# Performance work log

Measured on AMD Instinct MI355X. Metric: run time of the kernel, lower is better.

The kernel has to match this reference:

```python
import jax, jax.numpy as jnp
import numpy as np

B, N, D = 2, 256, 256  # module only type-checks when n_tokens == dim
EPS = 1e-5


def _ln(x, gamma, beta):
    m = jnp.mean(x, axis=-1, keepdims=True)
    v = jnp.var(x, axis=-1, keepdims=True)
    return (x - m) * jax.lax.rsqrt(v + EPS) * gamma + beta


def setup_inputs() -> dict:
    key = jax.random.key(0)
    k0, k1, k2, k3 = jax.random.split(key, 4)
    s = 1.0 / np.sqrt(D).astype(np.float32)
    return {
        "pair_repr": jax.random.normal(k0, (B, N, N, D), jnp.float32),
        "w_in": jax.random.normal(k1, (2 * D, D), jnp.float32) * s,
        "w_gate": jax.random.normal(k2, (D, D), jnp.float32) * s,
        "w_out": jax.random.normal(k3, (D, D), jnp.float32) * s,
        "ln_gamma": jnp.ones((D,), jnp.float32),
        "ln_beta": jnp.zeros((D,), jnp.float32),
    }


def reference(pair_repr, w_in, w_gate, w_out, ln_gamma, ln_beta):
    # shared LayerNorm applied to input
    x = _ln(pair_repr, ln_gamma, ln_beta)                      # [B,N,N,D]
    ab = jnp.einsum('bnid,ed->bnie', x, w_in)                  # [B,N,N,2D]
    a, b = jnp.split(ab, 2, axis=-1)
    a = jax.nn.sigmoid(a) * a                                  # SiLU
    b = jax.nn.sigmoid(b) * b
    g = jax.nn.sigmoid(jnp.einsum('bnid,ed->bnie', x, w_gate))  # [B,N,N,D]
    # 'incoming' pattern: torch.einsum('...ki,...kj->...ij') with ellipsis = (B, N);
    # contracts over the second token axis k, i/j index the channel axis (needs N == D).
    tri = jnp.einsum('bnki,bnkj->bnij', a, b)                  # [B,N,D,D]
    out = jnp.einsum('bnij,ej->bnie', _ln(tri, ln_gamma, ln_beta), w_out)
    return out * g
```

## Files before the change

kernel.cpp:

```cpp
#include <hip/hip_runtime.h>
#include <hip/hip_bf16.h>

typedef __attribute__((ext_vector_type(4))) float  f32x4;
typedef __attribute__((ext_vector_type(8))) short  s16x8;
typedef __attribute__((ext_vector_type(4))) short  s16x4;

union BH4 { s16x4 v; __hip_bfloat16 h[4]; };
union BH8 { s16x8 v; __hip_bfloat16 h[8]; };

#define MFMA16(A,B,C) __builtin_amdgcn_mfma_f32_16x16x32_bf16((A),(B),(C),0,0,0)

__device__ __forceinline__ float sigm(float x) { return 1.0f / (1.0f + __expf(-x)); }

__device__ __forceinline__ int xad(int r, int byteInRow) {
  return ((r << 9) + byteInRow) ^ ((r & 7) << 4);
}
__device__ __forceinline__ int cad64(int i, int k) {
  return (i << 7) + ((((k >> 3) ^ (i & 7)) << 4) | ((k & 7) << 1));
}

__global__ void wfrag_kernel(const float* __restrict__ w_in,
                             const float* __restrict__ w_gate,
                             const float* __restrict__ w_out,
                             __hip_bfloat16* __restrict__ dst) {
  const int lane = threadIdx.x;
  const int fid  = blockIdx.x;
  const int m    = blockIdx.y;
  const float* src = (m == 0) ? w_in : (m == 1) ? (w_in + 65536)
                    : (m == 2) ? w_gate : w_out;
  const int e  = (fid >> 3) * 16 + (lane & 15);
  const int d0 = (fid & 7) * 32 + (lane >> 4) * 8;
  BH8 u;
  #pragma unroll
  for (int j = 0; j < 8; ++j) u.h[j] = __float2bfloat16(src[e * 256 + d0 + j]);
  *reinterpret_cast<s16x8*>(dst + (size_t)m * 65536 + ((size_t)fid * 64 + lane) * 8) = u.v;
}

__global__ __launch_bounds__(512, 4) void k2_lnabg(
    const float* __restrict__ pair,
    const __hip_bfloat16* __restrict__ wfrag,
    const float* __restrict__ gamma, const float* __restrict__ beta,
    __hip_bfloat16* __restrict__ aT, __hip_bfloat16* __restrict__ bT,
    __hip_bfloat16* __restrict__ gws)
{
  __shared__ __align__(16) char lds[65536];
  const int raw = blockIdx.x;
  const int s   = (raw & 7) * 64 + (raw >> 3);
  const int tid = threadIdx.x, lane = tid & 63, w = tid >> 6;
  const int l15 = lane & 15, lh = lane >> 4;
  char* const XW = lds + w * 8192;

  const float4 gm = *reinterpret_cast<const float4*>(gamma + lane * 4);
  const float4 bt = *reinterpret_cast<const float4*>(beta  + lane * 4);

  s16x8 xr[2][8];
  #pragma unroll
  for (int rt = 0; rt < 2; ++rt) {
    #pragma unroll 1
    for (int rr = 0; rr < 16; ++rr) {
      const int r = w * 32 + rt * 16 + rr;
      const float4 v = *reinterpret_cast<const float4*>(
          pair + ((size_t)s * 256 + r) * 256 + lane * 4);
      float sm = v.x + v.y + v.z + v.w;
      float ss = v.x*v.x + v.y*v.y + v.z*v.z + v.w*v.w;
      #pragma unroll
      for (int m = 1; m < 64; m <<= 1) { sm += __shfl_xor(sm, m); ss += __shfl_xor(ss, m); }
      const float mean = sm * (1.f/256.f);
      const float rstd = rsqrtf(ss * (1.f/256.f) - mean*mean + 1e-5f);
      BH4 o;
      o.h[0] = __float2bfloat16((v.x - mean) * rstd * gm.x + bt.x);
      o.h[1] = __float2bfloat16((v.y - mean) * rstd * gm.y + bt.y);
      o.h[2] = __float2bfloat16((v.z - mean) * rstd * gm.z + bt.z);
      o.h[3] = __float2bfloat16((v.w - mean) * rstd * gm.w + bt.w);
      *reinterpret_cast<s16x4*>(XW + xad(rr, lane * 8)) = o.v;
    }
    #pragma unroll
    for (int ks = 0; ks < 8; ++ks)
      xr[rt][ks] = *reinterpret_cast<const s16x8*>(XW + xad(l15, ks*64 + lh*16));
  }

  #pragma unroll 1
  for (int cg = 0; cg < 48; ++cg) {
    const int m  = cg >> 4;
    const int ct = cg & 15;
    f32x4 acc0 = (f32x4){0.f,0.f,0.f,0.f};
    f32x4 acc1 = (f32x4){0.f,0.f,0.f,0.f};
    #pragma unroll
    for (int ks = 0; ks < 8; ++ks) {
      const s16x8 Bf = *reinterpret_cast<const s16x8*>(
          wfrag + ((size_t)cg * 8 + ks) * 512 + lane * 8);
      acc0 = MFMA16(xr[0][ks], Bf, acc0);
      acc1 = MFMA16(xr[1][ks], Bf, acc1);
    }
    if (m < 2) {
      __hip_bfloat16* const dst = (m == 0) ? aT : bT;
      #pragma unroll
      for (int rt = 0; rt < 2; ++rt) {
        const f32x4 a = rt ? acc1 : acc0;
        BH4 o;
        #pragma unroll
        for (int q = 0; q < 4; ++q) o.h[q] = __float2bfloat16(a[q] * sigm(a[q]));
        const int lane2 = l15 + 16 * ((rt*2 + (lh >> 1)) & 3);
        *reinterpret_cast<s16x4*>(
            dst + (((size_t)s*16 + ct)*8 + w)*512 + lane2*8 + (lh & 1)*4) = o.v;
      }
    } else {
      #pragma unroll
      for (int rt = 0; rt < 2; ++rt) {
        const f32x4 a = rt ? acc1 : acc0;
        BH4 o;
        #pragma unroll
        for (int q = 0; q < 4; ++q) o.h[q] = __float2bfloat16(sigm(a[q]));
        const int rtg = w * 2 + rt;
        *reinterpret_cast<s16x4*>(
            gws + (((size_t)s*16 + rtg)*16 + ct)*256 + lane*4) = o.v;
      }
    }
  }
}

__global__ __launch_bounds__(512, 4) void k3_tri(
    const __hip_bfloat16* __restrict__ aT, const __hip_bfloat16* __restrict__ bT,
    const __hip_bfloat16* __restrict__ gws, const __hip_bfloat16* __restrict__ wfrag,
    const float* __restrict__ gamma, const float* __restrict__ beta,
    float* __restrict__ out)
{
  extern __shared__ __align__(16) char lds[];
  char*  const STG = lds;
  char*  const SW  = lds;
  float* const ST  = (float*)(lds + 65536);

  const int raw = blockIdx.x;
  const int s   = (raw & 7) * 64 + ((raw >> 3) >> 1);
  const int h   = (raw >> 3) & 1;
  const int tid = threadIdx.x, lane = tid & 63, w = tid >> 6;
  const int l15 = lane & 15, lh = lane >> 4;
  const int r2 = w >> 1, ch = w & 1;

  f32x4 tri[2][8];
  #pragma unroll
  for (int rt = 0; rt < 2; ++rt)
    #pragma unroll
    for (int t = 0; t < 8; ++t) tri[rt][t] = (f32x4){0.f,0.f,0.f,0.f};

  const int f0 = w * 3;
  s16x8 stg[3];
  #pragma unroll
  for (int p = 0; p < 3; ++p) {
    const int f = f0 + p;
    const __hip_bfloat16* src = (f < 8)
        ? aT + (((size_t)s*16 + h*8 + f)*8 + 0)*512
        : bT + (((size_t)s*16 + (f-8))*8 + 0)*512;
    stg[p] = *reinterpret_cast<const s16x8*>(src + lane*8);
  }

  for (int c = 0; c < 8; ++c) {
    #pragma unroll
    for (int p = 0; p < 3; ++p)
      *reinterpret_cast<s16x8*>(STG + (f0 + p)*1024 + lane*16) = stg[p];
    __syncthreads();
    if (c < 7) {
      #pragma unroll
      for (int p = 0; p < 3; ++p) {
        const int f = f0 + p;
        const __hip_bfloat16* src = (f < 8)
            ? aT + (((size_t)s*16 + h*8 + f)*8 + (c+1))*512
            : bT + (((size_t)s*16 + (f-8))*8 + (c+1))*512;
        stg[p] = *reinterpret_cast<const s16x8*>(src + lane*8);
      }
    }
    const s16x8 ta0 = *reinterpret_cast<const s16x8*>(STG + (r2*2+0)*1024 + lane*16);
    const s16x8 ta1 = *reinterpret_cast<const s16x8*>(STG + (r2*2+1)*1024 + lane*16);
    #pragma unroll
    for (int t = 0; t < 8; ++t) {
      const s16x8 tb = *reinterpret_cast<const s16x8*>(
          STG + (8 + ch*8 + t)*1024 + lane*16);
      tri[0][t] = MFMA16(ta0, tb, tri[0][t]);
      tri[1][t] = MFMA16(ta1, tb, tri[1][t]);
    }
    __syncthreads();
  }

  float psm[2][4], pss[2][4];
  #pragma unroll
  for (int rt = 0; rt < 2; ++rt)
    #pragma unroll
    for (int q = 0; q < 4; ++q) {
      float sm = 0.f, ss = 0.f;
      #pragma unroll
      for (int t = 0; t < 8; ++t) { const float v = tri[rt][t][q]; sm += v; ss += v*v; }
      #pragma unroll
      for (int m = 1; m < 16; m <<= 1) { sm += __shfl_xor(sm, m); ss += __shfl_xor(ss, m); }
      psm[rt][q] = sm; pss[rt][q] = ss;
    }
  if (l15 == 0) {
    #pragma unroll
    for (int rt = 0; rt < 2; ++rt)
      #pragma unroll
      for (int q = 0; q < 4; ++q) {
        const int idx = ((w*2 + rt)*4 + lh)*4 + q;
        ST[idx*2 + 0] = psm[rt][q];
        ST[idx*2 + 1] = pss[rt][q];
      }
  }
  __syncthreads();
  float mean[2][4], rstd[2][4];
  #pragma unroll
  for (int rt = 0; rt < 2; ++rt)
    #pragma unroll
    for (int q = 0; q < 4; ++q) {
      const int idx = (((w ^ 1)*2 + rt)*4 + lh)*4 + q;
      const float sm = psm[rt][q] + ST[idx*2 + 0];
      const float ss = pss[rt][q] + ST[idx*2 + 1];
      mean[rt][q] = sm * (1.f/256.f);
      rstd[rt][q] = rsqrtf(ss * (1.f/256.f) - mean[rt][q]*mean[rt][q] + 1e-5f);
    }
  __syncthreads();
  #pragma unroll
  for (int t = 0; t < 8; ++t) {
    const int j = (ch*8 + t)*16 + l15;
    const float gmv = gamma[j], btv = beta[j];
    #pragma unroll
    for (int rt = 0; rt < 2; ++rt)
      #pragma unroll
      for (int q = 0; q < 4; ++q) {
        const int iloc = r2*32 + rt*16 + lh*4 + q;
        const float v = (tri[rt][t][q] - mean[rt][q]) * rstd[rt][q] * gmv + btv;
        *reinterpret_cast<__hip_bfloat16*>(SW + xad(iloc, j*2)) = __float2bfloat16(v);
      }
  }
  __syncthreads();

  const __hip_bfloat16* const wo = wfrag + 196608;
  f32x4 oo[2][8];
  #pragma unroll
  for (int rt = 0; rt < 2; ++rt)
    #pragma unroll
    for (int t = 0; t < 8; ++t) oo[rt][t] = (f32x4){0.f,0.f,0.f,0.f};
  #pragma unroll
  for (int ks = 0; ks < 8; ++ks) {
    const s16x8 A0 = *reinterpret_cast<const s16x8*>(
        SW + xad(r2*32 +  0 + l15, ks*64 + lh*16));
    const s16x8 A1 = *reinterpret_cast<const s16x8*>(
        SW + xad(r2*32 + 16 + l15, ks*64 + lh*16));
    #pragma unroll
    for (int t = 0; t < 8; ++t) {
      const int cte = ch*8 + t;
      const s16x8 Bo = *reinterpret_cast<const s16x8*>(
          wo + ((size_t)(cte*8 + ks))*512 + lane*8);
      oo[0][t] = MFMA16(A0, Bo, oo[0][t]);
      oo[1][t] = MFMA16(A1, Bo, oo[1][t]);
    }
  }
  #pragma unroll
  for (int rt = 0; rt < 2; ++rt) {
    const int rtg = h*8 + r2*2 + rt;
    #pragma unroll
    for (int t = 0; t < 8; ++t) {
      BH4 gv;
      gv.v = *reinterpret_cast<const s16x4*>(
          gws + (((size_t)s*16 + rtg)*16 + (ch*8 + t))*256 + lane*4);
      #pragma unroll
      for (int q = 0; q < 4; ++q) {
        const int row = h*128 + r2*32 + rt*16 + lh*4 + q;
        out[((size_t)s*256 + row)*256 + (ch*8 + t)*16 + l15] =
            oo[rt][t][q] * __bfloat162float(gv.h[q]);
      }
    }
  }
}

__global__ __launch_bounds__(256) void ln_kernel(
    const float* __restrict__ pair, const float* __restrict__ gamma,
    const float* __restrict__ beta, __hip_bfloat16* __restrict__ xws)
{
  __shared__ char Xl[8192];
  const int t  = threadIdx.x;
  const int s  = blockIdx.x >> 4;
  const int rt = blockIdx.x & 15;
  const int r  = t >> 4;
  const int c0 = (t & 15) * 16;
  const float* src = pair + (((size_t)s * 256 + rt * 16 + r) * 256 + c0);
  float v[16];
  #pragma unroll
  for (int i = 0; i < 4; ++i) {
    const float4 f = *reinterpret_cast<const float4*>(src + i * 4);
    v[i*4+0]=f.x; v[i*4+1]=f.y; v[i*4+2]=f.z; v[i*4+3]=f.w;
  }
  float sm = 0.f, ss = 0.f;
  #pragma unroll
  for (int i = 0; i < 16; ++i) { sm += v[i]; ss += v[i]*v[i]; }
  #pragma unroll
  for (int m = 1; m < 16; m <<= 1) { sm += __shfl_xor(sm, m); ss += __shfl_xor(ss, m); }
  const float mean = sm * (1.f/256.f);
  const float rstd = rsqrtf(ss * (1.f/256.f) - mean*mean + 1e-5f);
  #pragma unroll
  for (int i = 0; i < 4; ++i) {
    const float4 gm = *reinterpret_cast<const float4*>(gamma + c0 + i*4);
    const float4 bt = *reinterpret_cast<const float4*>(beta  + c0 + i*4);
    BH4 o;
    o.h[0] = __float2bfloat16((v[i*4+0]-mean)*rstd*gm.x + bt.x);
    o.h[1] = __float2bfloat16((v[i*4+1]-mean)*rstd*gm.y + bt.y);
    o.h[2] = __float2bfloat16((v[i*4+2]-mean)*rstd*gm.z + bt.z);
    o.h[3] = __float2bfloat16((v[i*4+3]-mean)*rstd*gm.w + bt.w);
    *reinterpret_cast<s16x4*>(Xl + xad(r, (c0 + i*4)*2)) = o.v;
  }
  __syncthreads();
  #pragma unroll
  for (int p = 0; p < 2; ++p) {
    const int u  = t + p * 256;
    const int ks = u >> 6;
    const int lp = u & 63;
    const s16x8 f = *reinterpret_cast<const s16x8*>(
        Xl + xad(lp & 15, ks*64 + ((lp>>4)&3)*16));
    *reinterpret_cast<s16x8*>(xws + ((((size_t)s*16 + rt)*8 + ks)*64 + lp)*8) = f;
  }
}

__global__ __launch_bounds__(512, 2) void tri_fused_fb(
    const __hip_bfloat16* __restrict__ xws,
    const __hip_bfloat16* __restrict__ wfrag,
    const float* __restrict__ gamma, const float* __restrict__ beta,
    float* __restrict__ out)
{
  extern __shared__ __align__(16) char lds[];
  char* const XS = lds;
  char* const AC = lds + 32768;
  char* const BC = lds + 49152;
  char* const SW = lds;

  const int raw = blockIdx.x;
  const int xcd = raw & 7, o = raw >> 3;
  const int s   = xcd * 64 + (o >> 1);
  const int h   = o & 1;

  const int tid = threadIdx.x, lane = tid & 63, w = tid >> 6;
  const int l15 = lane & 15, lh = lane >> 4;

  const __hip_bfloat16* const wa = wfrag;
  const __hip_bfloat16* const wb = wfrag + 65536;
  const __hip_bfloat16* const wg = wfrag + 131072;
  const __hip_bfloat16* const wo = wfrag + 196608;
  const __hip_bfloat16* const xs = xws + (size_t)s * 65536;
  const char* const xsb = (const char*)xs;

  f32x4 tri[16];
  #pragma unroll
  for (int jt = 0; jt < 16; ++jt) tri[jt] = (f32x4){0.f,0.f,0.f,0.f};

  {
    s16x8 st[4];
    #pragma unroll
    for (int p = 0; p < 4; ++p)
      st[p] = *reinterpret_cast<const s16x8*>(xsb + p*8192 + tid*16);
    #pragma unroll
    for (int p = 0; p < 4; ++p)
      *reinterpret_cast<s16x8*>(XS + p*8192 + tid*16) = st[p];
  }
  __syncthreads();

  for (int c = 0; c < 4; ++c) {
    {
      const int ct = h*8 + w;
      f32x4 acc[4];
      #pragma unroll
      for (int rt = 0; rt < 4; ++rt) acc[rt] = (f32x4){0.f,0.f,0.f,0.f};
      #pragma unroll
      for (int ks = 0; ks < 8; ++ks) {
        const s16x8 Bf = *reinterpret_cast<const s16x8*>(wa + (((size_t)ct*8 + ks)*64 + lane)*8);
        #pragma unroll
        for (int rt = 0; rt < 4; ++rt) {
// ... 84 lines not shown
    }
  }
  __syncthreads();

  #pragma unroll
  for (int half = 0; half < 2; ++half) {
    #pragma unroll
    for (int t = 0; t < 2; ++t) {
      const int ct = 2*w + t;
      f32x4 og[4], oo[4];
      #pragma unroll
      for (int rt = 0; rt < 4; ++rt) { og[rt] = (f32x4){0.f,0.f,0.f,0.f}; oo[rt] = (f32x4){0.f,0.f,0.f,0.f}; }
      #pragma unroll
      for (int ks = 0; ks < 8; ++ks) {
        const s16x8 Bg = *reinterpret_cast<const s16x8*>(wg + (((size_t)ct*8 + ks)*64 + lane)*8);
        const s16x8 Bo = *reinterpret_cast<const s16x8*>(wo + (((size_t)ct*8 + ks)*64 + lane)*8);
        #pragma unroll
        for (int rt = 0; rt < 4; ++rt) {
          const int rtg = h*8 + half*4 + rt;
          const s16x8 Ax  = *reinterpret_cast<const s16x8*>(xs + (((size_t)rtg*8 + ks)*64 + lane)*8);
          const s16x8 Aln = *reinterpret_cast<const s16x8*>(
              SW + xad(half*64 + rt*16 + l15, ks*64 + lh*16));
          og[rt] = MFMA16(Ax,  Bg, og[rt]);
          oo[rt] = MFMA16(Aln, Bo, oo[rt]);
        }
      }
      #pragma unroll
      for (int rt = 0; rt < 4; ++rt) {
        #pragma unroll
        for (int q = 0; q < 4; ++q) {
          const int row = h*128 + half*64 + rt*16 + lh*4 + q;
          out[(size_t)s*65536 + (size_t)row*256 + ct*16 + l15] =
              oo[rt][q] * sigm(og[rt][q]);
        }
      }
    }
  }
}

extern "C" void kernel_launch(void* const* d_in, const int* in_sizes, int n_in,
                              void* d_out, int out_size, void* d_ws, size_t ws_size,
                              hipStream_t stream) {
  const float* pair   = (const float*)d_in[0];
  const float* w_in   = (const float*)d_in[1];
  const float* w_gate = (const float*)d_in[2];
  const float* w_out  = (const float*)d_in[3];
  const float* gamma  = (const float*)d_in[4];
  const float* beta   = (const float*)d_in[5];
  float* out = (float*)d_out;

  (void)in_sizes; (void)n_in; (void)out_size;

  __hip_bfloat16* wfrag = (__hip_bfloat16*)d_ws;

  wfrag_kernel<<<dim3(128, 4), 64, 0, stream>>>(w_in, w_gate, w_out, wfrag);

  if (ws_size >= 201850880ULL) {
    __hip_bfloat16* aT  = (__hip_bfloat16*)((char*)d_ws + 524288);
    __hip_bfloat16* bT  = (__hip_bfloat16*)((char*)d_ws + 524288 + 67108864);
    __hip_bfloat16* gws = (__hip_bfloat16*)((char*)d_ws + 524288 + 2*67108864);
    hipFuncSetAttribute(reinterpret_cast<const void*>(k3_tri),
                        hipFuncAttributeMaxDynamicSharedMemorySize, 67584);
    k2_lnabg<<<512, 512, 0, stream>>>(pair, wfrag, gamma, beta, aT, bT, gws);
    k3_tri<<<1024, 512, 67584, stream>>>(aT, bT, gws, wfrag, gamma, beta, out);
  } else {
    __hip_bfloat16* xws = (__hip_bfloat16*)((char*)d_ws + 524288);
    hipFuncSetAttribute(reinterpret_cast<const void*>(tri_fused_fb),
                        hipFuncAttributeMaxDynamicSharedMemorySize, 81920);
    ln_kernel<<<8192, 256, 0, stream>>>(pair, gamma, beta, xws);
    tri_fused_fb<<<1024, 512, 81920, stream>>>(xws, wfrag, gamma, beta, out);
  }
}
```

Measured before the change: 239.6 us.

## Split LayerNorm into its own kernel and recompute gate inside tri kernel

The LayerNorm is moved out of the a/b projection kernel into a separate ln_kernel that writes bf16 fragments once. The gate projection is no longer materialised as a bf16 buffer; k3_tri recomputes it with MFMAs from the normalized input, fused with the output projection. k2_ab now double-buffers weight fragments in LDS with a prefetch, replacing direct global loads. This trades a 32 MB gate write and read for an extra 32 MB xws write and read, plus more MFMA work in k3 and an extra kernel launch.

```diff
diff --git a/kernel.cpp b/kernel.cpp
--- a/kernel.cpp
+++ b/kernel.cpp
@@ -36,240 +36,6 @@
   *reinterpret_cast<s16x8*>(dst + (size_t)m * 65536 + ((size_t)fid * 64 + lane) * 8) = u.v;
 }
 
-__global__ __launch_bounds__(512, 4) void k2_lnabg(
-    const float* __restrict__ pair,
-    const __hip_bfloat16* __restrict__ wfrag,
-    const float* __restrict__ gamma, const float* __restrict__ beta,
-    __hip_bfloat16* __restrict__ aT, __hip_bfloat16* __restrict__ bT,
-    __hip_bfloat16* __restrict__ gws)
-{
-  __shared__ __align__(16) char lds[65536];
-  const int raw = blockIdx.x;
-  const int s   = (raw & 7) * 64 + (raw >> 3);
-  const int tid = threadIdx.x, lane = tid & 63, w = tid >> 6;
-  const int l15 = lane & 15, lh = lane >> 4;
-  char* const XW = lds + w * 8192;
-
-  const float4 gm = *reinterpret_cast<const float4*>(gamma + lane * 4);
-  const float4 bt = *reinterpret_cast<const float4*>(beta  + lane * 4);
-
-  s16x8 xr[2][8];
-  #pragma unroll
-  for (int rt = 0; rt < 2; ++rt) {
-    #pragma unroll 1
-    for (int rr = 0; rr < 16; ++rr) {
-      const int r = w * 32 + rt * 16 + rr;
-      const float4 v = *reinterpret_cast<const float4*>(
-          pair + ((size_t)s * 256 + r) * 256 + lane * 4);
-      float sm = v.x + v.y + v.z + v.w;
-      float ss = v.x*v.x + v.y*v.y + v.z*v.z + v.w*v.w;
-      #pragma unroll
-      for (int m = 1; m < 64; m <<= 1) { sm += __shfl_xor(sm, m); ss += __shfl_xor(ss, m); }
-      const float mean = sm * (1.f/256.f);
-      const float rstd = rsqrtf(ss * (1.f/256.f) - mean*mean + 1e-5f);
-      BH4 o;
-      o.h[0] = __float2bfloat16((v.x - mean) * rstd * gm.x + bt.x);
-      o.h[1] = __float2bfloat16((v.y - mean) * rstd * gm.y + bt.y);
-      o.h[2] = __float2bfloat16((v.z - mean) * rstd * gm.z + bt.z);
-      o.h[3] = __float2bfloat16((v.w - mean) * rstd * gm.w + bt.w);
-      *reinterpret_cast<s16x4*>(XW + xad(rr, lane * 8)) = o.v;
-    }
-    #pragma unroll
-    for (int ks = 0; ks < 8; ++ks)
-      xr[rt][ks] = *reinterpret_cast<const s16x8*>(XW + xad(l15, ks*64 + lh*16));
-  }
-
-  #pragma unroll 1
-  for (int cg = 0; cg < 48; ++cg) {
-    const int m  = cg >> 4;
-    const int ct = cg & 15;
-    f32x4 acc0 = (f32x4){0.f,0.f,0.f,0.f};
-    f32x4 acc1 = (f32x4){0.f,0.f,0.f,0.f};
-    #pragma unroll
-    for (int ks = 0; ks < 8; ++ks) {
-      const s16x8 Bf = *reinterpret_cast<const s16x8*>(
-          wfrag + ((size_t)cg * 8 + ks) * 512 + lane * 8);
-      acc0 = MFMA16(xr[0][ks], Bf, acc0);
-      acc1 = MFMA16(xr[1][ks], Bf, acc1);
-    }
-    if (m < 2) {
-      __hip_bfloat16* const dst = (m == 0) ? aT : bT;
-      #pragma unroll
-      for (int rt = 0; rt < 2; ++rt) {
-        const f32x4 a = rt ? acc1 : acc0;
-        BH4 o;
-        #pragma unroll
-        for (int q = 0; q < 4; ++q) o.h[q] = __float2bfloat16(a[q] * sigm(a[q]));
-        const int lane2 = l15 + 16 * ((rt*2 + (lh >> 1)) & 3);
-        *reinterpret_cast<s16x4*>(
-            dst + (((size_t)s*16 + ct)*8 + w)*512 + lane2*8 + (lh & 1)*4) = o.v;
-      }
-    } else {
-      #pragma unroll
-      for (int rt = 0; rt < 2; ++rt) {
-        const f32x4 a = rt ? acc1 : acc0;
-        BH4 o;
-        #pragma unroll
-        for (int q = 0; q < 4; ++q) o.h[q] = __float2bfloat16(sigm(a[q]));
-        const int rtg = w * 2 + rt;
-        *reinterpret_cast<s16x4*>(
-            gws + (((size_t)s*16 + rtg)*16 + ct)*256 + lane*4) = o.v;
-      }
-    }
-  }
-}
-
-__global__ __launch_bounds__(512, 4) void k3_tri(
-    const __hip_bfloat16* __restrict__ aT, const __hip_bfloat16* __restrict__ bT,
-    const __hip_bfloat16* __restrict__ gws, const __hip_bfloat16* __restrict__ wfrag,
-    const float* __restrict__ gamma, const float* __restrict__ beta,
-    float* __restrict__ out)
-{
-  extern __shared__ __align__(16) char lds[];
-  char*  const STG = lds;
-  char*  const SW  = lds;
-  float* const ST  = (float*)(lds + 65536);
-
-  const int raw = blockIdx.x;
-  const int s   = (raw & 7) * 64 + ((raw >> 3) >> 1);
-  const int h   = (raw >> 3) & 1;
-  const int tid = threadIdx.x, lane = tid & 63, w = tid >> 6;
-  const int l15 = lane & 15, lh = lane >> 4;
-  const int r2 = w >> 1, ch = w & 1;
-
-  f32x4 tri[2][8];
-  #pragma unroll
-  for (int rt = 0; rt < 2; ++rt)
-    #pragma unroll
-    for (int t = 0; t < 8; ++t) tri[rt][t] = (f32x4){0.f,0.f,0.f,0.f};
-
-  const int f0 = w * 3;
-  s16x8 stg[3];
-  #pragma unroll
-  for (int p = 0; p < 3; ++p) {
-    const int f = f0 + p;
-    const __hip_bfloat16* src = (f < 8)
-        ? aT + (((size_t)s*16 + h*8 + f)*8 + 0)*512
-        : bT + (((size_t)s*16 + (f-8))*8 + 0)*512;
-    stg[p] = *reinterpret_cast<const s16x8*>(src + lane*8);
-  }
-
-  for (int c = 0; c < 8; ++c) {
-    #pragma unroll
-    for (int p = 0; p < 3; ++p)
-      *reinterpret_cast<s16x8*>(STG + (f0 + p)*1024 + lane*16) = stg[p];
-    __syncthreads();
-    if (c < 7) {
-      #pragma unroll
-      for (int p = 0; p < 3; ++p) {
-        const int f = f0 + p;
-        const __hip_bfloat16* src = (f < 8)
-            ? aT + (((size_t)s*16 + h*8 + f)*8 + (c+1))*512
-            : bT + (((size_t)s*16 + (f-8))*8 + (c+1))*512;
-        stg[p] = *reinterpret_cast<const s16x8*>(src + lane*8);
-      }
-    }
-    const s16x8 ta0 = *reinterpret_cast<const s16x8*>(STG + (r2*2+0)*1024 + lane*16);
-    const s16x8 ta1 = *reinterpret_cast<const s16x8*>(STG + (r2*2+1)*1024 + lane*16);
-    #pragma unroll
-    for (int t = 0; t < 8; ++t) {
-      const s16x8 tb = *reinterpret_cast<const s16x8*>(
-          STG + (8 + ch*8 + t)*1024 + lane*16);
-      tri[0][t] = MFMA16(ta0, tb, tri[0][t]);
-      tri[1][t] = MFMA16(ta1, tb, tri[1][t]);
-    }
-    __syncthreads();
-  }
-
-  float psm[2][4], pss[2][4];
-  #pragma unroll
-  for (int rt = 0; rt < 2; ++rt)
-    #pragma unroll
-    for (int q = 0; q < 4; ++q) {
-      float sm = 0.f, ss = 0.f;
-      #pragma unroll
-      for (int t = 0; t < 8; ++t) { const float v = tri[rt][t][q]; sm += v; ss += v*v; }
-      #pragma unroll
-      for (int m = 1; m < 16; m <<= 1) { sm += __shfl_xor(sm, m); ss += __shfl_xor(ss, m); }
-      psm[rt][q] = sm; pss[rt][q] = ss;
-    }
-  if (l15 == 0) {
-    #pragma unroll
-    for (int rt = 0; rt < 2; ++rt)
-      #pragma unroll
-      for (int q = 0; q < 4; ++q) {
-        const int idx = ((w*2 + rt)*4 + lh)*4 + q;
-        ST[idx*2 + 0] = psm[rt][q];
-        ST[idx*2 + 1] = pss[rt][q];
-      }
-  }
-  __syncthreads();
-  float mean[2][4], rstd[2][4];
-  #pragma unroll
-  for (int rt = 0; rt < 2; ++rt)
-    #pragma unroll
-    for (int q = 0; q < 4; ++q) {
-      const int idx = (((w ^ 1)*2 + rt)*4 + lh)*4 + q;
-      const float sm = psm[rt][q] + ST[idx*2 + 0];
-      const float ss = pss[rt][q] + ST[idx*2 + 1];
-      mean[rt][q] = sm * (1.f/256.f);
-      rstd[rt][q] = rsqrtf(ss * (1.f/256.f) - mean[rt][q]*mean[rt][q] + 1e-5f);
-    }
-  __syncthreads();
-  #pragma unroll
-  for (int t = 0; t < 8; ++t) {
-    const int j = (ch*8 + t)*16 + l15;
-    const float gmv = gamma[j], btv = beta[j];
-    #pragma unroll
-    for (int rt = 0; rt < 2; ++rt)
-      #pragma unroll
-      for (int q = 0; q < 4; ++q) {
-        const int iloc = r2*32 + rt*16 + lh*4 + q;
-        const float v = (tri[rt][t][q] - mean[rt][q]) * rstd[rt][q] * gmv + btv;
-        *reinterpret_cast<__hip_bfloat16*>(SW + xad(iloc, j*2)) = __float2bfloat16(v);
-      }
-  }
-  __syncthreads();
-
-  const __hip_bfloat16* const wo = wfrag + 196608;
-  f32x4 oo[2][8];
-  #pragma unroll
-  for (int rt = 0; rt < 2; ++rt)
-    #pragma unroll
-    for (int t = 0; t < 8; ++t) oo[rt][t] = (f32x4){0.f,0.f,0.f,0.f};
-  #pragma unroll
-  for (int ks = 0; ks < 8; ++ks) {
-    const s16x8 A0 = *reinterpret_cast<const s16x8*>(
-        SW + xad(r2*32 +  0 + l15, ks*64 + lh*16));
-    const s16x8 A1 = *reinterpret_cast<const s16x8*>(
-        SW + xad(r2*32 + 16 + l15, ks*64 + lh*16));
-    #pragma unroll
-    for (int t = 0; t < 8; ++t) {
-      const int cte = ch*8 + t;
-      const s16x8 Bo = *reinterpret_cast<const s16x8*>(
-          wo + ((size_t)(cte*8 + ks))*512 + lane*8);
-      oo[0][t] = MFMA16(A0, Bo, oo[0][t]);
-      oo[1][t] = MFMA16(A1, Bo, oo[1][t]);
-    }
-  }
-  #pragma unroll
-  for (int rt = 0; rt < 2; ++rt) {
-    const int rtg = h*8 + r2*2 + rt;
-    #pragma unroll
-    for (int t = 0; t < 8; ++t) {
-      BH4 gv;
-      gv.v = *reinterpret_cast<const s16x4*>(
-          gws + (((size_t)s*16 + rtg)*16 + (ch*8 + t))*256 + lane*4);
-      #pragma unroll
-      for (int q = 0; q < 4; ++q) {
-        const int row = h*128 + r2*32 + rt*16 + lh*4 + q;
-        out[((size_t)s*256 + row)*256 + (ch*8 + t)*16 + l15] =
-            oo[rt][t][q] * __bfloat162float(gv.h[q]);
-      }
-    }
-  }
-}
-
 __global__ __launch_bounds__(256) void ln_kernel(
     const float* __restrict__ pair, const float* __restrict__ gamma,
     const float* __restrict__ beta, __hip_bfloat16* __restrict__ xws)
@@ -317,6 +83,224 @@
   }
 }
 
+__global__ __launch_bounds__(512, 4) void k2_ab(
+    const __hip_bfloat16* __restrict__ xws,
+    const __hip_bfloat16* __restrict__ wfrag,
+    __hip_bfloat16* __restrict__ aT, __hip_bfloat16* __restrict__ bT)
+{
+  __shared__ __align__(16) char wb2[2][8192];
+  const int raw = blockIdx.x;
+  const int s   = (raw & 7) * 64 + (raw >> 3);
+  const int tid = threadIdx.x, lane = tid & 63, w = tid >> 6;
+  const int l15 = lane & 15, lh = lane >> 4;
+
+  s16x8 xr[2][8];
+  #pragma unroll
+  for (int rt = 0; rt < 2; ++rt)
+    #pragma unroll
+    for (int ks = 0; ks < 8; ++ks)
+      xr[rt][ks] = *reinterpret_cast<const s16x8*>(
+          xws + (((size_t)s*16 + (w*2 + rt))*8 + ks)*512 + lane*8);
+
+  {
+    const s16x8 v0 = *reinterpret_cast<const s16x8*>(wfrag + tid*8);
+    *reinterpret_cast<s16x8*>(&wb2[0][tid*16]) = v0;
+  }
+  __syncthreads();
+
+  #pragma unroll 1
+  for (int cg = 0; cg < 32; ++cg) {
+    const int cur = cg & 1;
+    s16x8 pf;
+    if (cg < 31)
+      pf = *reinterpret_cast<const s16x8*>(wfrag + (size_t)(cg+1)*4096 + tid*8);
+
+    const int m  = cg >> 4;
+    const int ct = cg & 15;
+    f32x4 acc0 = (f32x4){0.f,0.f,0.f,0.f};
+    f32x4 acc1 = (f32x4){0.f,0.f,0.f,0.f};
+    #pragma unroll
+    for (int ks = 0; ks < 8; ++ks) {
+      const s16x8 Bf = *reinterpret_cast<const s16x8*>(&wb2[cur][ks*1024 + lane*16]);
+      acc0 = MFMA16(xr[0][ks], Bf, acc0);
+      acc1 = MFMA16(xr[1][ks], Bf, acc1);
+    }
+    __hip_bfloat16* const dst = (m == 0) ? aT : bT;
+    #pragma unroll
+    for (int rt = 0; rt < 2; ++rt) {
+      const f32x4 a = rt ? acc1 : acc0;
+      BH4 o;
+      #pragma unroll
+      for (int q = 0; q < 4; ++q) o.h[q] = __float2bfloat16(a[q] * sigm(a[q]));
+      const int lane2 = l15 + 16 * ((rt*2 + (lh >> 1)) & 3);
+      *reinterpret_cast<s16x4*>(
+          dst + (((size_t)s*16 + ct)*8 + w)*512 + lane2*8 + (lh & 1)*4) = o.v;
+    }
+    if (cg < 31)
+      *reinterpret_cast<s16x8*>(&wb2[cur ^ 1][tid*16]) = pf;
+    __syncthreads();
+  }
+}
+
+__global__ __launch_bounds__(512, 4) void k3_tri(
+    const __hip_bfloat16* __restrict__ aT, const __hip_bfloat16* __restrict__ bT,
+    const __hip_bfloat16* __restrict__ xws, const __hip_bfloat16* __restrict__ wfrag,
+    const float* __restrict__ gamma, const float* __restrict__ beta,
+    float* __restrict__ out)
+{
+  extern __shared__ __align__(16) char lds[];
+  char*  const STG = lds;
+  char*  const SW  = lds;
+  float* const ST  = (float*)(lds + 65536);
+
+  const int raw = blockIdx.x;
+  const int s   = (raw & 7) * 64 + ((raw >> 3) >> 1);
+  const int h   = (raw >> 3) & 1;
+  const int tid = threadIdx.x, lane = tid & 63, w = tid >> 6;
+  const int l15 = lane & 15, lh = lane >> 4;
+  const int r2 = w >> 1, ch = w & 1;
+
+  f32x4 tri[2][8];
+  #pragma unroll
+  for (int rt = 0; rt < 2; ++rt)
+    #pragma unroll
+    for (int t = 0; t < 8; ++t) tri[rt][t] = (f32x4){0.f,0.f,0.f,0.f};
+
+  const int f0 = w * 3;
+  s16x8 stg[3];
+  #pragma unroll
+  for (int p = 0; p < 3; ++p) {
+    const int f = f0 + p;
+    const __hip_bfloat16* src = (f < 8)
+        ? aT + (((size_t)s*16 + h*8 + f)*8 + 0)*512
+        : bT + (((size_t)s*16 + (f-8))*8 + 0)*512;
+    stg[p] = *reinterpret_cast<const s16x8*>(src + lane*8);
+  }
+
+  for (int c = 0; c < 8; ++c) {
+    #pragma unroll
+    for (int p = 0; p < 3; ++p)
+      *reinterpret_cast<s16x8*>(STG + (f0 + p)*1024 + lane*16) = stg[p];
+    __syncthreads();
+    if (c < 7) {
+      #pragma unroll
+      for (int p = 0; p < 3; ++p) {
+        const int f = f0 + p;
+        const __hip_bfloat16* src = (f < 8)
+            ? aT + (((size_t)s*16 + h*8 + f)*8 + (c+1))*512
+            : bT + (((size_t)s*16 + (f-8))*8 + (c+1))*512;
+        stg[p] = *reinterpret_cast<const s16x8*>(src + lane*8);
+      }
+    }
+    const s16x8 ta0 = *reinterpret_cast<const s16x8*>(STG + (r2*2+0)*1024 + lane*16);
+    const s16x8 ta1 = *reinterpret_cast<const s16x8*>(STG + (r2*2+1)*1024 + lane*16);
+    #pragma unroll
+    for (int t = 0; t < 8; ++t) {
+      const s16x8 tb = *reinterpret_cast<const s16x8*>(
+          STG + (8 + ch*8 + t)*1024 + lane*16);
+      tri[0][t] = MFMA16(ta0, tb, tri[0][t]);
+      tri[1][t] = MFMA16(ta1, tb, tri[1][t]);
+    }
+    __syncthreads();
+  }
+
+  float psm[2][4], pss[2][4];
+  #pragma unroll
+  for (int rt = 0; rt < 2; ++rt)
+    #pragma unroll
+    for (int q = 0; q < 4; ++q) {
+      float sm = 0.f, ss = 0.f;
+      #pragma unroll
+      for (int t = 0; t < 8; ++t) { const float v = tri[rt][t][q]; sm += v; ss += v*v; }
+      #pragma unroll
+      for (int m = 1; m < 16; m <<= 1) { sm += __shfl_xor(sm, m); ss += __shfl_xor(ss, m); }
+      psm[rt][q] = sm; pss[rt][q] = ss;
+    }
+  if (l15 == 0) {
+    #pragma unroll
+    for (int rt = 0; rt < 2; ++rt)
+      #pragma unroll
+      for (int q = 0; q < 4; ++q) {
+        const int idx = ((w*2 + rt)*4 + lh)*4 + q;
+        ST[idx*2 + 0] = psm[rt][q];
+        ST[idx*2 + 1] = pss[rt][q];
+      }
+  }
+  __syncthreads();
+  float mean[2][4], rstd[2][4];
+  #pragma unroll
+  for (int rt = 0; rt < 2; ++rt)
+    #pragma unroll
+    for (int q = 0; q < 4; ++q) {
+      const int idx = (((w ^ 1)*2 + rt)*4 + lh)*4 + q;
+      const float sm = psm[rt][q] + ST[idx*2 + 0];
+      const float ss = pss[rt][q] + ST[idx*2 + 1];
+      mean[rt][q] = sm * (1.f/256.f);
+      rstd[rt][q] = rsqrtf(ss * (1.f/256.f) - mean[rt][q]*mean[rt][q] + 1e-5f);
+    }
+  __syncthreads();
+  #pragma unroll
+  for (int t = 0; t < 8; ++t) {
+    const int j = (ch*8 + t)*16 + l15;
+    const float gmv = gamma[j], btv = beta[j];
+    #pragma unroll
+    for (int rt = 0; rt < 2; ++rt)
+      #pragma unroll
+      for (int q = 0; q < 4; ++q) {
+        const int iloc = r2*32 + rt*16 + lh*4 + q;
+        const float v = (tri[rt][t][q] - mean[rt][q]) * rstd[rt][q] * gmv + btv;
+        *reinterpret_cast<__hip_bfloat16*>(SW + xad(iloc, j*2)) = __float2bfloat16(v);
+      }
+  }
+  __syncthreads();
+
+  const __hip_bfloat16* const wg = wfrag + 131072;
+  const __hip_bfloat16* const wo = wfrag + 196608;
+  #pragma unroll 1
+  for (int th = 0; th < 2; ++th) {
+    f32x4 og[2][4], oo[2][4];
+    #pragma unroll
+    for (int rt = 0; rt < 2; ++rt)
+      #pragma unroll
+      for (int t = 0; t < 4; ++t) { og[rt][t] = (f32x4){0.f,0.f,0.f,0.f}; oo[rt][t] = (f32x4){0.f,0.f,0.f,0.f}; }
+    #pragma unroll
+    for (int ks = 0; ks < 8; ++ks) {
+      const s16x8 A0 = *reinterpret_cast<const s16x8*>(
+          SW + xad(r2*32 +  0 + l15, ks*64 + lh*16));
+      const s16x8 A1 = *reinterpret_cast<const s16x8*>(
+          SW + xad(r2*32 + 16 + l15, ks*64 + lh*16));
+      const s16x8 Ax0 = *reinterpret_cast<const s16x8*>(
+          xws + (((size_t)s*16 + (h*8 + r2*2 + 0))*8 + ks)*512 + lane*8);
+      const s16x8 Ax1 = *reinterpret_cast<const s16x8*>(
+          xws + (((size_t)s*16 + (h*8 + r2*2 + 1))*8 + ks)*512 + lane*8);
+      #pragma unroll
+      for (int t = 0; t < 4; ++t) {
+        const int cte = ch*8 + th*4 + t;
+        const s16x8 Bo = *reinterpret_cast<const s16x8*>(
+            wo + ((size_t)(cte*8 + ks))*512 + lane*8);
+        const s16x8 Bg = *reinterpret_cast<const s16x8*>(
+            wg + ((size_t)(cte*8 + ks))*512 + lane*8);
+        oo[0][t] = MFMA16(A0,  Bo, oo[0][t]);
+        oo[1][t] = MFMA16(A1,  Bo, oo[1][t]);
+        og[0][t] = MFMA16(Ax0, Bg, og[0][t]);
+        og[1][t] = MFMA16(Ax1, Bg, og[1][t]);
+      }
+    }
+    #pragma unroll
+    for (int rt = 0; rt < 2; ++rt) {
+      #pragma unroll
+      for (int t = 0; t < 4; ++t) {
+        #pragma unroll
+        for (int q = 0; q < 4; ++q) {
+          const int row = h*128 + r2*32 + rt*16 + lh*4 + q;
+          out[((size_t)s*256 + row)*256 + (ch*8 + th*4 + t)*16 + l15] =
+              oo[rt][t][q] * sigm(og[rt][t][q]);
+        }
+      }
+    }
+  }
+}
+
 __global__ __launch_bounds__(512, 2) void tri_fused_fb(
     const __hip_bfloat16* __restrict__ xws,
     const __hip_bfloat16* __restrict__ wfrag,
@@ -507,22 +491,21 @@
   (void)in_sizes; (void)n_in; (void)out_size;
 
   __hip_bfloat16* wfrag = (__hip_bfloat16*)d_ws;
+  __hip_bfloat16* xws   = (__hip_bfloat16*)((char*)d_ws + 524288);
 
   wfrag_kernel<<<dim3(128, 4), 64, 0, stream>>>(w_in, w_gate, w_out, wfrag);
+  ln_kernel<<<8192, 256, 0, stream>>>(pair, gamma, beta, xws);
 
   if (ws_size >= 201850880ULL) {
-    __hip_bfloat16* aT  = (__hip_bfloat16*)((char*)d_ws + 524288);
-    __hip_bfloat16* bT  = (__hip_bfloat16*)((char*)d_ws + 524288 + 67108864);
-    __hip_bfloat16* gws = (__hip_bfloat16*)((char*)d_ws + 524288 + 2*67108864);
+    __hip_bfloat16* aT = (__hip_bfloat16*)((char*)d_ws + 524288 + 67108864);
+    __hip_bfloat16* bT = (__hip_bfloat16*)((char*)d_ws + 524288 + 2*67108864);
     hipFuncSetAttribute(reinterpret_cast<const void*>(k3_tri),
                         hipFuncAttributeMaxDynamicSharedMemorySize, 67584);
-    k2_lnabg<<<512, 512, 0, stream>>>(pair, wfrag, gamma, beta, aT, bT, gws);
-    k3_tri<<<1024, 512, 67584, stream>>>(aT, bT, gws, wfrag, gamma, beta, out);
+    k2_ab<<<512, 512, 0, stream>>>(xws, wfrag, aT, bT);
+    k3_tri<<<1024, 512, 67584, stream>>>(aT, bT, xws, wfrag, gamma, beta, out);
   } else {
-    __hip_bfloat16* xws = (__hip_bfloat16*)((char*)d_ws + 524288);
     hipFuncSetAttribute(reinterpret_cast<const void*>(tri_fused_fb),
                         hipFuncAttributeMaxDynamicSharedMemorySize, 81920);
-    ln_kernel<<<8192, 256, 0, stream>>>(pair, gamma, beta, xws);
     tri_fused_fb<<<1024, 512, 81920, stream>>>(xws, wfrag, gamma, beta, out);
   }
 }
```

New measurement: 398.9 us. 66.5% more time.

## Split LayerNorm out of projection kernel, LDS-buffer weights, direct-load triangle operands

Applied to the files above, without the earlier changes.

LayerNorm now runs as its own kernel on every path, writing bf16 fragments to workspace. The projection kernel reads those fragments and double-buffers weight fragments through LDS with one barrier per column group. The triangle kernel drops its cooperative LDS staging and barriers and loads A/B fragments straight from global memory. The gate buffer aliases the LayerNorm workspace; each warp reads its own rows into registers before overwriting them. The extra launch and the bf16 write and read-back add memory traffic, which the simpler, barrier-free kernels are meant to offset.

```diff
diff --git a/kernel.cpp b/kernel.cpp
--- a/kernel.cpp
+++ b/kernel.cpp
@@ -36,240 +36,6 @@
   *reinterpret_cast<s16x8*>(dst + (size_t)m * 65536 + ((size_t)fid * 64 + lane) * 8) = u.v;
 }
 
-__global__ __launch_bounds__(512, 4) void k2_lnabg(
-    const float* __restrict__ pair,
-    const __hip_bfloat16* __restrict__ wfrag,
-    const float* __restrict__ gamma, const float* __restrict__ beta,
-    __hip_bfloat16* __restrict__ aT, __hip_bfloat16* __restrict__ bT,
-    __hip_bfloat16* __restrict__ gws)
-{
-  __shared__ __align__(16) char lds[65536];
-  const int raw = blockIdx.x;
-  const int s   = (raw & 7) * 64 + (raw >> 3);
-  const int tid = threadIdx.x, lane = tid & 63, w = tid >> 6;
-  const int l15 = lane & 15, lh = lane >> 4;
-  char* const XW = lds + w * 8192;
-
-  const float4 gm = *reinterpret_cast<const float4*>(gamma + lane * 4);
-  const float4 bt = *reinterpret_cast<const float4*>(beta  + lane * 4);
-
-  s16x8 xr[2][8];
-  #pragma unroll
-  for (int rt = 0; rt < 2; ++rt) {
-    #pragma unroll 1
-    for (int rr = 0; rr < 16; ++rr) {
-      const int r = w * 32 + rt * 16 + rr;
-      const float4 v = *reinterpret_cast<const float4*>(
-          pair + ((size_t)s * 256 + r) * 256 + lane * 4);
-      float sm = v.x + v.y + v.z + v.w;
-      float ss = v.x*v.x + v.y*v.y + v.z*v.z + v.w*v.w;
-      #pragma unroll
-      for (int m = 1; m < 64; m <<= 1) { sm += __shfl_xor(sm, m); ss += __shfl_xor(ss, m); }
-      const float mean = sm * (1.f/256.f);
-      const float rstd = rsqrtf(ss * (1.f/256.f) - mean*mean + 1e-5f);
-      BH4 o;
-      o.h[0] = __float2bfloat16((v.x - mean) * rstd * gm.x + bt.x);
-      o.h[1] = __float2bfloat16((v.y - mean) * rstd * gm.y + bt.y);
-      o.h[2] = __float2bfloat16((v.z - mean) * rstd * gm.z + bt.z);
-      o.h[3] = __float2bfloat16((v.w - mean) * rstd * gm.w + bt.w);
-      *reinterpret_cast<s16x4*>(XW + xad(rr, lane * 8)) = o.v;
-    }
-    #pragma unroll
-    for (int ks = 0; ks < 8; ++ks)
-      xr[rt][ks] = *reinterpret_cast<const s16x8*>(XW + xad(l15, ks*64 + lh*16));
-  }
-
-  #pragma unroll 1
-  for (int cg = 0; cg < 48; ++cg) {
-    const int m  = cg >> 4;
-    const int ct = cg & 15;
-    f32x4 acc0 = (f32x4){0.f,0.f,0.f,0.f};
-    f32x4 acc1 = (f32x4){0.f,0.f,0.f,0.f};
-    #pragma unroll
-    for (int ks = 0; ks < 8; ++ks) {
-      const s16x8 Bf = *reinterpret_cast<const s16x8*>(
-          wfrag + ((size_t)cg * 8 + ks) * 512 + lane * 8);
-      acc0 = MFMA16(xr[0][ks], Bf, acc0);
-      acc1 = MFMA16(xr[1][ks], Bf, acc1);
-    }
-    if (m < 2) {
-      __hip_bfloat16* const dst = (m == 0) ? aT : bT;
-      #pragma unroll
-      for (int rt = 0; rt < 2; ++rt) {
-        const f32x4 a = rt ? acc1 : acc0;
-        BH4 o;
-        #pragma unroll
-        for (int q = 0; q < 4; ++q) o.h[q] = __float2bfloat16(a[q] * sigm(a[q]));
-        const int lane2 = l15 + 16 * ((rt*2 + (lh >> 1)) & 3);
-        *reinterpret_cast<s16x4*>(
-            dst + (((size_t)s*16 + ct)*8 + w)*512 + lane2*8 + (lh & 1)*4) = o.v;
-      }
-    } else {
-      #pragma unroll
-      for (int rt = 0; rt < 2; ++rt) {
-        const f32x4 a = rt ? acc1 : acc0;
-        BH4 o;
-        #pragma unroll
-        for (int q = 0; q < 4; ++q) o.h[q] = __float2bfloat16(sigm(a[q]));
-        const int rtg = w * 2 + rt;
-        *reinterpret_cast<s16x4*>(
-            gws + (((size_t)s*16 + rtg)*16 + ct)*256 + lane*4) = o.v;
-      }
-    }
-  }
-}
-
-__global__ __launch_bounds__(512, 4) void k3_tri(
-    const __hip_bfloat16* __restrict__ aT, const __hip_bfloat16* __restrict__ bT,
-    const __hip_bfloat16* __restrict__ gws, const __hip_bfloat16* __restrict__ wfrag,
-    const float* __restrict__ gamma, const float* __restrict__ beta,
-    float* __restrict__ out)
-{
-  extern __shared__ __align__(16) char lds[];
-  char*  const STG = lds;
-  char*  const SW  = lds;
-  float* const ST  = (float*)(lds + 65536);
-
-  const int raw = blockIdx.x;
-  const int s   = (raw & 7) * 64 + ((raw >> 3) >> 1);
-  const int h   = (raw >> 3) & 1;
-  const int tid = threadIdx.x, lane = tid & 63, w = tid >> 6;
-  const int l15 = lane & 15, lh = lane >> 4;
-  const int r2 = w >> 1, ch = w & 1;
-
-  f32x4 tri[2][8];
-  #pragma unroll
-  for (int rt = 0; rt < 2; ++rt)
-    #pragma unroll
-    for (int t = 0; t < 8; ++t) tri[rt][t] = (f32x4){0.f,0.f,0.f,0.f};
-
-  const int f0 = w * 3;
-  s16x8 stg[3];
-  #pragma unroll
-  for (int p = 0; p < 3; ++p) {
-    const int f = f0 + p;
-    const __hip_bfloat16* src = (f < 8)
-        ? aT + (((size_t)s*16 + h*8 + f)*8 + 0)*512
-        : bT + (((size_t)s*16 + (f-8))*8 + 0)*512;
-    stg[p] = *reinterpret_cast<const s16x8*>(src + lane*8);
-  }
-
-  for (int c = 0; c < 8; ++c) {
-    #pragma unroll
-    for (int p = 0; p < 3; ++p)
-      *reinterpret_cast<s16x8*>(STG + (f0 + p)*1024 + lane*16) = stg[p];
-    __syncthreads();
-    if (c < 7) {
-      #pragma unroll
-      for (int p = 0; p < 3; ++p) {
-        const int f = f0 + p;
-        const __hip_bfloat16* src = (f < 8)
-            ? aT + (((size_t)s*16 + h*8 + f)*8 + (c+1))*512
-            : bT + (((size_t)s*16 + (f-8))*8 + (c+1))*512;
-        stg[p] = *reinterpret_cast<const s16x8*>(src + lane*8);
-      }
-    }
-    const s16x8 ta0 = *reinterpret_cast<const s16x8*>(STG + (r2*2+0)*1024 + lane*16);
-    const s16x8 ta1 = *reinterpret_cast<const s16x8*>(STG + (r2*2+1)*1024 + lane*16);
-    #pragma unroll
-    for (int t = 0; t < 8; ++t) {
-      const s16x8 tb = *reinterpret_cast<const s16x8*>(
-          STG + (8 + ch*8 + t)*1024 + lane*16);
-      tri[0][t] = MFMA16(ta0, tb, tri[0][t]);
-      tri[1][t] = MFMA16(ta1, tb, tri[1][t]);
-    }
-    __syncthreads();
-  }
-
-  float psm[2][4], pss[2][4];
-  #pragma unroll
-  for (int rt = 0; rt < 2; ++rt)
-    #pragma unroll
-    for (int q = 0; q < 4; ++q) {
-      float sm = 0.f, ss = 0.f;
-      #pragma unroll
-      for (int t = 0; t < 8; ++t) { const float v = tri[rt][t][q]; sm += v; ss += v*v; }
-      #pragma unroll
-      for (int m = 1; m < 16; m <<= 1) { sm += __shfl_xor(sm, m); ss += __shfl_xor(ss, m); }
-      psm[rt][q] = sm; pss[rt][q] = ss;
-    }
-  if (l15 == 0) {
-    #pragma unroll
-    for (int rt = 0; rt < 2; ++rt)
-      #pragma unroll
-      for (int q = 0; q < 4; ++q) {
-        const int idx = ((w*2 + rt)*4 + lh)*4 + q;
-        ST[idx*2 + 0] = psm[rt][q];
-        ST[idx*2 + 1] = pss[rt][q];
-      }
-  }
-  __syncthreads();
-  float mean[2][4], rstd[2][4];
-  #pragma unroll
-  for (int rt = 0; rt < 2; ++rt)
-    #pragma unroll
-    for (int q = 0; q < 4; ++q) {
-      const int idx = (((w ^ 1)*2 + rt)*4 + lh)*4 + q;
-      const float sm = psm[rt][q] + ST[idx*2 + 0];
-      const float ss = pss[rt][q] + ST[idx*2 + 1];
-      mean[rt][q] = sm * (1.f/256.f);
-      rstd[rt][q] = rsqrtf(ss * (1.f/256.f) - mean[rt][q]*mean[rt][q] + 1e-5f);
-    }
-  __syncthreads();
-  #pragma unroll
-  for (int t = 0; t < 8; ++t) {
-    const int j = (ch*8 + t)*16 + l15;
-    const float gmv = gamma[j], btv = beta[j];
-    #pragma unroll
-    for (int rt = 0; rt < 2; ++rt)
-      #pragma unroll
-      for (int q = 0; q < 4; ++q) {
-        const int iloc = r2*32 + rt*16 + lh*4 + q;
-        const float v = (tri[rt][t][q] - mean[rt][q]) * rstd[rt][q] * gmv + btv;
-        *reinterpret_cast<__hip_bfloat16*>(SW + xad(iloc, j*2)) = __float2bfloat16(v);
-      }
-  }
-  __syncthreads();
-
-  const __hip_bfloat16* const wo = wfrag + 196608;
-  f32x4 oo[2][8];
-  #pragma unroll
-  for (int rt = 0; rt < 2; ++rt)
-    #pragma unroll
-    for (int t = 0; t < 8; ++t) oo[rt][t] = (f32x4){0.f,0.f,0.f,0.f};
-  #pragma unroll
-  for (int ks = 0; ks < 8; ++ks) {
-    const s16x8 A0 = *reinterpret_cast<const s16x8*>(
-        SW + xad(r2*32 +  0 + l15, ks*64 + lh*16));
-    const s16x8 A1 = *reinterpret_cast<const s16x8*>(
-        SW + xad(r2*32 + 16 + l15, ks*64 + lh*16));
-    #pragma unroll
-    for (int t = 0; t < 8; ++t) {
-      const int cte = ch*8 + t;
-      const s16x8 Bo = *reinterpret_cast<const s16x8*>(
-          wo + ((size_t)(cte*8 + ks))*512 + lane*8);
-      oo[0][t] = MFMA16(A0, Bo, oo[0][t]);
-      oo[1][t] = MFMA16(A1, Bo, oo[1][t]);
-    }
-  }
-  #pragma unroll
-  for (int rt = 0; rt < 2; ++rt) {
-    const int rtg = h*8 + r2*2 + rt;
-    #pragma unroll
-    for (int t = 0; t < 8; ++t) {
-      BH4 gv;
-      gv.v = *reinterpret_cast<const s16x4*>(
-          gws + (((size_t)s*16 + rtg)*16 + (ch*8 + t))*256 + lane*4);
-      #pragma unroll
-      for (int q = 0; q < 4; ++q) {
-        const int row = h*128 + r2*32 + rt*16 + lh*4 + q;
-        out[((size_t)s*256 + row)*256 + (ch*8 + t)*16 + l15] =
-            oo[rt][t][q] * __bfloat162float(gv.h[q]);
-      }
-    }
-  }
-}
-
 __global__ __launch_bounds__(256) void ln_kernel(
     const float* __restrict__ pair, const float* __restrict__ gamma,
     const float* __restrict__ beta, __hip_bfloat16* __restrict__ xws)
@@ -317,6 +83,206 @@
   }
 }
 
+__global__ __launch_bounds__(512, 4) void k2_abg(
+    const __hip_bfloat16* __restrict__ xws,
+    const __hip_bfloat16* __restrict__ wfrag,
+    __hip_bfloat16* __restrict__ aT, __hip_bfloat16* __restrict__ bT,
+    __hip_bfloat16* __restrict__ gws)
+{
+  __shared__ __align__(16) char wb2[2][8192];
+  const int raw = blockIdx.x;
+  const int s   = (raw & 7) * 64 + (raw >> 3);
+  const int tid = threadIdx.x, lane = tid & 63, w = tid >> 6;
+  const int l15 = lane & 15, lh = lane >> 4;
+
+  s16x8 xr[2][8];
+  #pragma unroll
+  for (int rt = 0; rt < 2; ++rt)
+    #pragma unroll
+    for (int ks = 0; ks < 8; ++ks)
+      xr[rt][ks] = *reinterpret_cast<const s16x8*>(
+          xws + (((size_t)s*16 + (w*2 + rt))*8 + ks)*512 + lane*8);
+
+  {
+    const s16x8 v0 = *reinterpret_cast<const s16x8*>(wfrag + tid*8);
+    *reinterpret_cast<s16x8*>(&wb2[0][tid*16]) = v0;
+  }
+  __syncthreads();
+
+  #pragma unroll 1
+  for (int cg = 0; cg < 48; ++cg) {
+    const int cur = cg & 1;
+    s16x8 pf;
+    if (cg < 47)
+      pf = *reinterpret_cast<const s16x8*>(wfrag + (size_t)(cg+1)*4096 + tid*8);
+
+    const int m  = cg >> 4;
+    const int ct = cg & 15;
+    f32x4 acc0 = (f32x4){0.f,0.f,0.f,0.f};
+    f32x4 acc1 = (f32x4){0.f,0.f,0.f,0.f};
+    #pragma unroll
+    for (int ks = 0; ks < 8; ++ks) {
+      const s16x8 Bf = *reinterpret_cast<const s16x8*>(&wb2[cur][ks*1024 + lane*16]);
+      acc0 = MFMA16(xr[0][ks], Bf, acc0);
+      acc1 = MFMA16(xr[1][ks], Bf, acc1);
+    }
+    if (m < 2) {
+      __hip_bfloat16* const dst = (m == 0) ? aT : bT;
+      #pragma unroll
+      for (int rt = 0; rt < 2; ++rt) {
+        const f32x4 a = rt ? acc1 : acc0;
+        BH4 o;
+        #pragma unroll
+        for (int q = 0; q < 4; ++q) o.h[q] = __float2bfloat16(a[q] * sigm(a[q]));
+        const int lane2 = l15 + 16 * ((rt*2 + (lh >> 1)) & 3);
+        *reinterpret_cast<s16x4*>(
+            dst + (((size_t)s*16 + ct)*8 + w)*512 + lane2*8 + (lh & 1)*4) = o.v;
+      }
+    } else {
+      #pragma unroll
+      for (int rt = 0; rt < 2; ++rt) {
+        const f32x4 a = rt ? acc1 : acc0;
+        BH4 o;
+        #pragma unroll
+        for (int q = 0; q < 4; ++q) o.h[q] = __float2bfloat16(sigm(a[q]));
+        const int rtg = w * 2 + rt;
+        *reinterpret_cast<s16x4*>(
+            gws + (((size_t)s*16 + rtg)*16 + ct)*256 + lane*4) = o.v;
+      }
+    }
+    if (cg < 47)
+      *reinterpret_cast<s16x8*>(&wb2[cur ^ 1][tid*16]) = pf;
+    __syncthreads();
+  }
+}
+
+__global__ __launch_bounds__(512, 4) void k3_tri(
+    const __hip_bfloat16* __restrict__ aT, const __hip_bfloat16* __restrict__ bT,
+    const __hip_bfloat16* __restrict__ gws, const __hip_bfloat16* __restrict__ wfrag,
+    const float* __restrict__ gamma, const float* __restrict__ beta,
+    float* __restrict__ out)
+{
+  __shared__ __align__(16) char lds[65536];
+  char*  const SW = lds;
+  float* const ST = (float*)lds;
+
+  const int raw = blockIdx.x;
+  const int s   = (raw & 7) * 64 + ((raw >> 3) >> 1);
+  const int h   = (raw >> 3) & 1;
+  const int tid = threadIdx.x, lane = tid & 63, w = tid >> 6;
+  const int l15 = lane & 15, lh = lane >> 4;
+  const int r2 = w >> 1, ch = w & 1;
+
+  f32x4 tri[2][8];
+  #pragma unroll
+  for (int rt = 0; rt < 2; ++rt)
+    #pragma unroll
+    for (int t = 0; t < 8; ++t) tri[rt][t] = (f32x4){0.f,0.f,0.f,0.f};
+
+  const __hip_bfloat16* const a0b = aT + ((size_t)s*16 + h*8 + r2*2 + 0)*8*512 + lane*8;
+  const __hip_bfloat16* const a1b = aT + ((size_t)s*16 + h*8 + r2*2 + 1)*8*512 + lane*8;
+  const __hip_bfloat16* const bbb = bT + ((size_t)s*16 + ch*8)*8*512 + lane*8;
+
+  #pragma unroll 1
+  for (int c = 0; c < 8; ++c) {
+    const s16x8 ta0 = *reinterpret_cast<const s16x8*>(a0b + (size_t)c*512);
+    const s16x8 ta1 = *reinterpret_cast<const s16x8*>(a1b + (size_t)c*512);
+    #pragma unroll
+    for (int t = 0; t < 8; ++t) {
+      const s16x8 tb = *reinterpret_cast<const s16x8*>(bbb + ((size_t)t*8 + c)*512);
+      tri[0][t] = MFMA16(ta0, tb, tri[0][t]);
+      tri[1][t] = MFMA16(ta1, tb, tri[1][t]);
+    }
+  }
+
+  float psm[2][4], pss[2][4];
+  #pragma unroll
+  for (int rt = 0; rt < 2; ++rt)
+    #pragma unroll
+    for (int q = 0; q < 4; ++q) {
+      float sm = 0.f, ss = 0.f;
+      #pragma unroll
+      for (int t = 0; t < 8; ++t) { const float v = tri[rt][t][q]; sm += v; ss += v*v; }
+      #pragma unroll
+      for (int m = 1; m < 16; m <<= 1) { sm += __shfl_xor(sm, m); ss += __shfl_xor(ss, m); }
+      psm[rt][q] = sm; pss[rt][q] = ss;
+    }
+  if (l15 == 0) {
+    #pragma unroll
+    for (int rt = 0; rt < 2; ++rt)
+      #pragma unroll
+      for (int q = 0; q < 4; ++q) {
+        const int idx = ((w*2 + rt)*4 + lh)*4 + q;
+        ST[idx*2 + 0] = psm[rt][q];
+        ST[idx*2 + 1] = pss[rt][q];
+      }
+  }
+  __syncthreads();
+  float mean[2][4], rstd[2][4];
+  #pragma unroll
+  for (int rt = 0; rt < 2; ++rt)
+    #pragma unroll
+    for (int q = 0; q < 4; ++q) {
+      const int idx = (((w ^ 1)*2 + rt)*4 + lh)*4 + q;
+      const float sm = psm[rt][q] + ST[idx*2 + 0];
+      const float ss = pss[rt][q] + ST[idx*2 + 1];
+      mean[rt][q] = sm * (1.f/256.f);
+      rstd[rt][q] = rsqrtf(ss * (1.f/256.f) - mean[rt][q]*mean[rt][q] + 1e-5f);
+    }
+  __syncthreads();
+  #pragma unroll
+  for (int t = 0; t < 8; ++t) {
+    const int j = (ch*8 + t)*16 + l15;
+    const float gmv = gamma[j], btv = beta[j];
+    #pragma unroll
+    for (int rt = 0; rt < 2; ++rt)
+      #pragma unroll
+      for (int q = 0; q < 4; ++q) {
+        const int iloc = r2*32 + rt*16 + lh*4 + q;
+        const float v = (tri[rt][t][q] - mean[rt][q]) * rstd[rt][q] * gmv + btv;
+        *reinterpret_cast<__hip_bfloat16*>(SW + xad(iloc, j*2)) = __float2bfloat16(v);
+      }
+  }
+  __syncthreads();
+
+  const __hip_bfloat16* const wo = wfrag + 196608;
+  f32x4 oo[2][8];
+  #pragma unroll
+  for (int rt = 0; rt < 2; ++rt)
+    #pragma unroll
+    for (int t = 0; t < 8; ++t) oo[rt][t] = (f32x4){0.f,0.f,0.f,0.f};
+  #pragma unroll
+  for (int ks = 0; ks < 8; ++ks) {
+    const s16x8 A0 = *reinterpret_cast<const s16x8*>(
+        SW + xad(r2*32 +  0 + l15, ks*64 + lh*16));
+    const s16x8 A1 = *reinterpret_cast<const s16x8*>(
+        SW + xad(r2*32 + 16 + l15, ks*64 + lh*16));
+    #pragma unroll
+    for (int t = 0; t < 8; ++t) {
+      const s16x8 Bo = *reinterpret_cast<const s16x8*>(
+          wo + ((size_t)((ch*8 + t)*8 + ks))*512 + lane*8);
+      oo[0][t] = MFMA16(A0, Bo, oo[0][t]);
+      oo[1][t] = MFMA16(A1, Bo, oo[1][t]);
+    }
+  }
+  #pragma unroll
+  for (int rt = 0; rt < 2; ++rt) {
+    const int rtg = h*8 + r2*2 + rt;
+    #pragma unroll
+    for (int t = 0; t < 8; ++t) {
+      BH4 gv;
+      gv.v = *reinterpret_cast<const s16x4*>(
+          gws + (((size_t)s*16 + rtg)*16 + (ch*8 + t))*256 + lane*4);
+      #pragma unroll
+      for (int q = 0; q < 4; ++q) {
+        const int row = h*128 + r2*32 + rt*16 + lh*4 + q;
+        out[((size_t)s*256 + row)*256 + (ch*8 + t)*16 + l15] =
+            oo[rt][t][q] * __bfloat162float(gv.h[q]);
+      }
+    }
+  }
+}
+
 __global__ __launch_bounds__(512, 2) void tri_fused_fb(
     const __hip_bfloat16* __restrict__ xws,
     const __hip_bfloat16* __restrict__ wfrag,
@@ -507,22 +473,20 @@
   (void)in_sizes; (void)n_in; (void)out_size;
 
   __hip_bfloat16* wfrag = (__hip_bfloat16*)d_ws;
+  __hip_bfloat16* xws   = (__hip_bfloat16*)((char*)d_ws + 524288);
 
   wfrag_kernel<<<dim3(128, 4), 64, 0, stream>>>(w_in, w_gate, w_out, wfrag);
+  ln_kernel<<<8192, 256, 0, stream>>>(pair, gamma, beta, xws);
 
   if (ws_size >= 201850880ULL) {
-    __hip_bfloat16* aT  = (__hip_bfloat16*)((char*)d_ws + 524288);
-    __hip_bfloat16* bT  = (__hip_bfloat16*)((char*)d_ws + 524288 + 67108864);
-    __hip_bfloat16* gws = (__hip_bfloat16*)((char*)d_ws + 524288 + 2*67108864);
-    hipFuncSetAttribute(reinterpret_cast<const void*>(k3_tri),
-                        hipFuncAttributeMaxDynamicSharedMemorySize, 67584);
-    k2_lnabg<<<512, 512, 0, stream>>>(pair, wfrag, gamma, beta, aT, bT, gws);
-    k3_tri<<<1024, 512, 67584, stream>>>(aT, bT, gws, wfrag, gamma, beta, out);
+    __hip_bfloat16* aT  = (__hip_bfloat16*)((char*)d_ws + 524288 + 67108864);
+    __hip_bfloat16* bT  = (__hip_bfloat16*)((char*)d_ws + 524288 + 2*67108864);
+    __hip_bfloat16* gws = xws;
+    k2_abg<<<512, 512, 0, stream>>>(xws, wfrag, aT, bT, gws);
+    k3_tri<<<1024, 512, 0, stream>>>(aT, bT, gws, wfrag, gamma, beta, out);
   } else {
-    __hip_bfloat16* xws = (__hip_bfloat16*)((char*)d_ws + 524288);
     hipFuncSetAttribute(reinterpret_cast<const void*>(tri_fused_fb),
                         hipFuncAttributeMaxDynamicSharedMemorySize, 81920);
-    ln_kernel<<<8192, 256, 0, stream>>>(pair, gamma, beta, xws);
     tri_fused_fb<<<1024, 512, 81920, stream>>>(xws, wfrag, gamma, beta, out);
   }
 }
```

After: 229.2 us. 1.05x faster.
